# Optimization experiments

Hardware: AMD Instinct MI355X
Metric: run time of the kernel (lower is better)

Reference implementation:

```python
import jax, jax.numpy as jnp
import numpy as np

EMB, NH, NG, T_MAX = 2048, 16, 4, 2048
HD = EMB // NH          # 128
HPG = NH // NG          # 4
B, T = 2, 2048


def _rope_tables(t):
    inv_freq = 1.0 / (10000.0 ** (jnp.arange(0, HD, 2, dtype=jnp.float32) / HD))
    freqs = jnp.outer(jnp.arange(t, dtype=jnp.float32), inv_freq)  # [t, HD//2]
    return jnp.cos(freqs), jnp.sin(freqs)


def _apply_rope(x, cos, sin):
    # x: [..., t, HD], interleaved pairs (0::2 real, 1::2 imag)
    x1 = x[..., 0::2]
    x2 = x[..., 1::2]
    r1 = x1 * cos - x2 * sin
    r2 = x1 * sin + x2 * cos
    return jnp.stack([r1, r2], axis=-1).reshape(x.shape)


def setup_inputs() -> dict:
    key = jax.random.key(0)
    ks = jax.random.split(key, 5)
    s = 0.02
    return {
        "x": jax.random.normal(ks[0], (B, T, EMB), dtype=jnp.float32),
        "Wq": jax.random.normal(ks[1], (EMB, EMB), dtype=jnp.float32) * s,
        "Wk": jax.random.normal(ks[2], (NG * HD, EMB), dtype=jnp.float32) * s,
        "Wv": jax.random.normal(ks[3], (NG * HD, EMB), dtype=jnp.float32) * s,
        "Wo": jax.random.normal(ks[4], (EMB, EMB), dtype=jnp.float32) * s,
    }


def reference(x, Wq, Wk, Wv, Wo):
    b, t, _ = x.shape
    cos, sin = _rope_tables(t)  # [t, HD//2] each; broadcast over batch/heads

    # projections (torch Linear: x @ W.T)
    q = (x @ Wq.T).reshape(b, t, NH, HD).transpose(0, 2, 1, 3)  # [b, NH, t, HD]
    k = (x @ Wk.T).reshape(b, t, NG, HD).transpose(0, 2, 1, 3)  # [b, NG, t, HD]
    v = (x @ Wv.T).reshape(b, t, NG, HD).transpose(0, 2, 1, 3)  # [b, NG, t, HD]

    q = _apply_rope(q, cos, sin)
    k = _apply_rope(k, cos, sin)

    # grouped attention without materializing expanded K/V
    qg = q.reshape(b, NG, HPG, t, HD)                       # [b, g, h, t, d]
    scale = 1.0 / jnp.sqrt(jnp.asarray(HD, dtype=x.dtype))
    scores = jnp.einsum('bghtd,bgsd->bghts', qg, k) * scale  # [b, g, h, t, s]

    causal = jnp.tril(jnp.ones((t, t), dtype=bool))
    scores = jnp.where(causal, scores, jnp.finfo(scores.dtype).min)
    attn = jax.nn.softmax(scores, axis=-1)

    out = jnp.einsum('bghts,bgsd->bghtd', attn, v)           # [b, g, h, t, d]
    out = out.reshape(b, NH, t, HD).transpose(0, 2, 1, 3).reshape(b, t, EMB)
    return out @ Wo.T
```

## Files before the change

kernel.cpp:

```cpp
#include <hip/hip_runtime.h>
#include <stdint.h>
#include <math.h>

#define EMB 2048
#define NHq 16
#define NGk 4
#define HD 128
#define Bb 2
#define Tt 2048
#define MROWS (Bb*Tt)
#define QKVN 3072
#define NQT 32

typedef __bf16 bf16x8 __attribute__((ext_vector_type(8)));
typedef float f32x4 __attribute__((ext_vector_type(4)));
typedef unsigned short u16;
typedef unsigned int u32;

__device__ __forceinline__ u16 f2bf(float f) {
    unsigned int u = __float_as_uint(f);
    u += 0x7fff + ((u >> 16) & 1);
    return (u16)(u >> 16);
}

__device__ __forceinline__ u32 cvt_pk_bf16(float lo, float hi) {
    u32 r;
    asm("v_cvt_pk_bf16_f32 %0, %1, %2" : "=v"(r) : "v"(lo), "v"(hi));
    return r;
}

#define GLOAD_LDS16(g, l) \
    __builtin_amdgcn_global_load_lds((const __attribute__((address_space(1))) void*)(g), \
                                     (__attribute__((address_space(3))) void*)(l), 16, 0, 0)

__global__ void cast_bf16_kernel(const float* __restrict__ src, u16* __restrict__ dst, int n4) {
    int i = blockIdx.x * blockDim.x + threadIdx.x;
    if (i < n4) {
        float4 v = reinterpret_cast<const float4*>(src)[i];
        ushort4 o;
        o.x = f2bf(v.x); o.y = f2bf(v.y); o.z = f2bf(v.z); o.w = f2bf(v.w);
        reinterpret_cast<ushort4*>(dst)[i] = o;
    }
}

__global__ void rope_tables_kernel(float* __restrict__ ctab, float* __restrict__ stab) {
    int t = blockIdx.x, i = threadIdx.x;
    float inv = powf(10000.f, -2.f * (float)i / (float)HD);
    float ang = (float)t * inv;
    ctab[t * 64 + i] = cosf(ang);
    stab[t * 64 + i] = sinf(ang);
}

__global__ void rope_kernel(const float* __restrict__ lin, const float* __restrict__ ctab,
                            const float* __restrict__ stab, u16* __restrict__ out,
                            int coloff, int nh, float scale) {
    int i = threadIdx.x;
    int tt = blockIdx.x * 4 + threadIdx.y;
    int h = blockIdx.y, b = blockIdx.z;
    const float2 xv = *reinterpret_cast<const float2*>(
        &lin[((size_t)(b * Tt + tt)) * QKVN + coloff + h * HD + 2 * i]);
    float c = ctab[tt * 64 + i], s = stab[tt * 64 + i];
    ushort2 o;
    o.x = f2bf((xv.x * c - xv.y * s) * scale);
    o.y = f2bf((xv.x * s + xv.y * c) * scale);
    *reinterpret_cast<ushort2*>(&out[(((size_t)(b * nh + h)) * Tt + tt) * HD + 2 * i]) = o;
}

__global__ void vtrans_kernel(const float* __restrict__ lin, u16* __restrict__ vt) {
    int tx = threadIdx.x, dy = threadIdx.y;
    int tt = blockIdx.x * 64 + tx;
    int g = blockIdx.y, b = blockIdx.z;
    int ttp = (tt & ~31) | (((tt & 15) << 1) | ((tt >> 4) & 1));
    const float* src = &lin[((size_t)(b * Tt + tt)) * QKVN + EMB + NGk * HD + g * HD];
    u16* dst = &vt[(((size_t)(b * NGk + g)) * HD) * Tt + ttp];
    #pragma unroll
    for (int k = 0; k < 16; ++k) {
        int d = dy + k * 8;
        dst[(size_t)d * Tt] = f2bf(src[d]);
    }
}

__global__ __launch_bounds__(256) void gemm_bt(const u16* __restrict__ A, const u16* __restrict__ W,
                                               float* __restrict__ C, int M, int N, int K) {
    __shared__ u16 Atile[128 * 32];
    __shared__ u16 Btile[128 * 32];
    const int brow = blockIdx.x * 128;
    const int bcol = blockIdx.y * 128;
    const int t = threadIdx.x;
    const int w = t >> 6, l = t & 63;
    const int lr = l & 15, lq = l >> 4;
    const int wr = (w >> 1) * 64, wc = (w & 1) * 64;
    f32x4 acc[4][4] = {};
    const int nkt = K >> 5;
    for (int kt = 0; kt < nkt; ++kt) {
        const int k0 = kt * 32;
        #pragma unroll
        for (int i = 0; i < 2; ++i) {
            int f = i * 256 + t;
            int row = f >> 2, cb = (f & 3) * 8;
            GLOAD_LDS16(A + (size_t)(brow + row) * K + k0 + cb, &Atile[(i * 256 + w * 64) * 8]);
            GLOAD_LDS16(W + (size_t)(bcol + row) * K + k0 + cb, &Btile[(i * 256 + w * 64) * 8]);
        }
        __syncthreads();
        bf16x8 a[4], b[4];
        #pragma unroll
        for (int m = 0; m < 4; ++m)
            a[m] = *reinterpret_cast<const bf16x8*>(&Atile[(wr + m * 16 + lr) * 32 + lq * 8]);
        #pragma unroll
        for (int n = 0; n < 4; ++n)
            b[n] = *reinterpret_cast<const bf16x8*>(&Btile[(wc + n * 16 + lr) * 32 + lq * 8]);
        #pragma unroll
        for (int m = 0; m < 4; ++m)
            #pragma unroll
            for (int n = 0; n < 4; ++n)
                acc[m][n] = __builtin_amdgcn_mfma_f32_16x16x32_bf16(a[m], b[n], acc[m][n], 0, 0, 0);
        __syncthreads();
    }
    #pragma unroll
    for (int m = 0; m < 4; ++m)
        #pragma unroll
        for (int n = 0; n < 4; ++n)
            #pragma unroll
            for (int r = 0; r < 4; ++r)
                C[(size_t)(brow + wr + m * 16 + lq * 4 + r) * N + bcol + wc + n * 16 + lr] = acc[m][n][r];
}

__global__ __launch_bounds__(512) void flash_attn(const u16* __restrict__ Q, const u16* __restrict__ K,
                                                  const u16* __restrict__ Vt, u16* __restrict__ Out) {
    __shared__ __align__(16) char smem[73728];
    u16* KldsBase = (u16*)smem;
    u16* VldsBase = (u16*)(smem + 32768);
    const int ilo = blockIdx.x;
    const int ihi = NQT - 1 - ilo;
    const int h = blockIdx.y;
    const int b = blockIdx.z;
    const int g = h >> 2;
    const int t = threadIdx.x;
    const int w = t >> 6, l = t & 63;
    const int wq = w & 3, half = w >> 2;
    const int lr = l & 15, lq = l >> 4;
    char* Pw = smem + 65536 + w * 1024;

    const size_t qhead = ((size_t)(b * NHq + h)) * Tt;
    const size_t qblo = (qhead + ilo * 64 + wq * 16) * HD;
    const size_t qbhi = (qhead + ihi * 64 + wq * 16) * HD;
    bf16x8 qfl[4], qfh[4];
    #pragma unroll
    for (int d = 0; d < 4; ++d) {
        qfl[d] = *reinterpret_cast<const bf16x8*>(&Q[qblo + (size_t)lr * HD + d * 32 + lq * 8]);
        qfh[d] = *reinterpret_cast<const bf16x8*>(&Q[qbhi + (size_t)lr * HD + d * 32 + lq * 8]);
    }
    bf16x8 ones;
    #pragma unroll
    for (int j = 0; j < 8; ++j) ones[j] = (__bf16)1.0f;

    f32x4 ol[8] = {}, oh[8] = {};
    f32x4 lsl = {}, lsh = {};

    const int qlo0 = ilo * 64 + wq * 16 + lq * 4;
    const int qhi0 = ihi * 64 + wq * 16 + lq * 4;
    const size_t kbase  = ((size_t)(b * NGk + g)) * Tt * HD;
    const size_t vtbase = ((size_t)(b * NGk + g)) * HD * Tt;
    const int nkt = NQT - ilo;

    int kofs[2], vofs[2];
    #pragma unroll
    for (int j = 0; j < 2; ++j) {
        int krow = j * 32 + w * 4 + (l >> 4);
        kofs[j] = krow * HD + (((l & 15) ^ (krow & 7)) * 8);
        int vrow = j * 64 + w * 8 + (l >> 3);
        vofs[j] = vrow * (int)Tt + (((l & 7) ^ (vrow & 7)) * 8);
    }

    #pragma unroll
    for (int j = 0; j < 2; ++j) {
        GLOAD_LDS16(K + kbase + kofs[j], KldsBase + (j * 512 + w * 64) * 8);
        GLOAD_LDS16(Vt + vtbase + vofs[j], VldsBase + (j * 512 + w * 64) * 8);
    }
    int cur = 0;

    for (int kt = 0; kt < nkt; ++kt) {
        const int kp0 = kt * 64;
        __syncthreads();
        if (kt + 1 < nkt) {
            #pragma unroll
            for (int j = 0; j < 2; ++j) {
                GLOAD_LDS16(K + kbase + (size_t)(kp0 + 64) * HD + kofs[j],
                            KldsBase + (cur ^ 1) * 8192 + (j * 512 + w * 64) * 8);
                GLOAD_LDS16(Vt + vtbase + (kp0 + 64) + vofs[j],
                            VldsBase + (cur ^ 1) * 8192 + (j * 512 + w * 64) * 8);
            }
        }
        const char* Kb = smem + cur * 16384;
        const char* Vb = smem + 32768 + cur * 16384;

        const bool lo_act = (kt <= ilo);
        f32x4 sl[2] = {}, sh[2] = {};
        __builtin_amdgcn_s_setprio(1);
        #pragma unroll
        for (int ct = 0; ct < 2; ++ct) {
            #pragma unroll
            for (int d = 0; d < 4; ++d) {
                int row = half * 32 + ct * 16 + lr;
                int bo = row * 256 + ((d * 64 + lq * 16) ^ ((row & 7) << 4));
                bf16x8 kf = *reinterpret_cast<const bf16x8*>(Kb + bo);
                if (lo_act) sl[ct] = __builtin_amdgcn_mfma_f32_16x16x32_bf16(qfl[d], kf, sl[ct], 0, 0, 0);
                sh[ct] = __builtin_amdgcn_mfma_f32_16x16x32_bf16(qfh[d], kf, sh[ct], 0, 0, 0);
            }
        }
        __builtin_amdgcn_s_setprio(0);

        {
            const bool diag = (kt == nkt - 1);
            float e[2][4];
            #pragma unroll
            for (int ct = 0; ct < 2; ++ct)
                #pragma unroll
                for (int r = 0; r < 4; ++r) {
                    float v = sh[ct][r];
                    if (diag && (kp0 + half * 32 + ct * 16 + lr > qhi0 + r)) v = -1e30f;
                    e[ct][r] = exp2f(v);
                }
            #pragma unroll
            for (int r = 0; r < 4; ++r) {
                int row = lq * 4 + r;
                int bo = row * 64 + (((lr >> 2) ^ (row & 3)) << 4) + (lr & 3) * 4;
                *reinterpret_cast<u32*>(Pw + bo) = cvt_pk_bf16(e[0][r], e[1][r]);
            }
        }
        bf16x8 pfh = *reinterpret_cast<const bf16x8*>(Pw + lr * 64 + ((lq ^ (lr & 3)) << 4));
        bf16x8 pfl;
        if (lo_act) {
            const bool diag = (kt == ilo);
            float e[2][4];
            #pragma unroll
            for (int ct = 0; ct < 2; ++ct)
                #pragma unroll
                for (int r = 0; r < 4; ++r) {
                    float v = sl[ct][r];
                    if (diag && (kp0 + half * 32 + ct * 16 + lr > qlo0 + r)) v = -1e30f;
                    e[ct][r] = exp2f(v);
                }
            #pragma unroll
            for (int r = 0; r < 4; ++r) {
                int row = lq * 4 + r;
                int bo = row * 64 + (((lr >> 2) ^ (row & 3)) << 4) + (lr & 3) * 4;
                *reinterpret_cast<u32*>(Pw + bo) = cvt_pk_bf16(e[0][r], e[1][r]);
            }
            pfl = *reinterpret_cast<const bf16x8*>(Pw + lr * 64 + ((lq ^ (lr & 3)) << 4));
        }

        __builtin_amdgcn_s_setprio(1);
        #pragma unroll
        for (int n = 0; n < 8; ++n) {
            int vrow = n * 16 + lr;
            int bv = vrow * 128 + ((half * 64 + lq * 16) ^ ((vrow & 7) << 4));
            bf16x8 vf = *reinterpret_cast<const bf16x8*>(Vb + bv);
            oh[n] = __builtin_amdgcn_mfma_f32_16x16x32_bf16(pfh, vf, oh[n], 0, 0, 0);
            if (lo_act) ol[n] = __builtin_amdgcn_mfma_f32_16x16x32_bf16(pfl, vf, ol[n], 0, 0, 0);
        }
        lsh = __builtin_amdgcn_mfma_f32_16x16x32_bf16(pfh, ones, lsh, 0, 0, 0);
        if (lo_act) lsl = __builtin_amdgcn_mfma_f32_16x16x32_bf16(pfl, ones, lsl, 0, 0, 0);
        __builtin_amdgcn_s_setprio(0);
        cur ^= 1;
    }

    __syncthreads();
    float* Osh = (float*)smem;
    float* Lsh = (float*)(smem + 65536);
    if (half == 1) {
        #pragma unroll
        for (int n = 0; n < 8; ++n)
            #pragma unroll
            for (int r = 0; r < 4; ++r) {
                int row = lq * 4 + r, col = n * 16 + lr;
                Osh[(wq * 32 + row) * 128 + col] = oh[n][r];
                Osh[(wq * 32 + 16 + row) * 128 + col] = ol[n][r];
            }
        if (lr == 0) {
            #pragma unroll
            for (int r = 0; r < 4; ++r) {
                Lsh[wq * 32 + lq * 4 + r] = lsh[r];
                Lsh[wq * 32 + 16 + lq * 4 + r] = lsl[r];
            }
        }
    }
    __syncthreads();
    if (half == 0) {
        float invh[4], invl[4];
        #pragma unroll
        for (int r = 0; r < 4; ++r) {
            invh[r] = 1.f / (lsh[r] + Lsh[wq * 32 + lq * 4 + r]);
            invl[r] = 1.f / (lsl[r] + Lsh[wq * 32 + 16 + lq * 4 + r]);
        }
        const size_t obase = ((size_t)b * Tt) * EMB + (size_t)h * HD;
        #pragma unroll
        for (int n = 0; n < 8; ++n)
            #pragma unroll
            for (int r = 0; r < 4; ++r) {
                int row = lq * 4 + r, col = n * 16 + lr;
                float vh = oh[n][r] + Osh[(wq * 32 + row) * 128 + col];
                float vl = ol[n][r] + Osh[(wq * 32 + 16 + row) * 128 + col];
                int rh = ihi * 64 + wq * 16 + row;
                int rl = ilo * 64 + wq * 16 + row;
                Out[obase + (size_t)rh * EMB + col] = f2bf(vh * invh[r]);
                Out[obase + (size_t)rl * EMB + col] = f2bf(vl * invl[r]);
            }
    }
}

extern "C" void kernel_launch(void* const* d_in, const int* in_sizes, int n_in,
                              void* d_out, int out_size, void* d_ws, size_t ws_size,
                              hipStream_t stream) {
    (void)in_sizes; (void)n_in; (void)out_size; (void)ws_size;
    const float* x  = (const float*)d_in[0];
    const float* Wq = (const float*)d_in[1];
    const float* Wk = (const float*)d_in[2];
    const float* Wv = (const float*)d_in[3];
    const float* Wo = (const float*)d_in[4];
    float* out = (float*)d_out;

    char* ws = (char*)d_ws;
    size_t off = 0;
    auto alloc = [&](size_t bytes) { char* p = ws + off; off += (bytes + 255) & ~(size_t)255; return p; };

    u16* w_bf    = (u16*)alloc((size_t)(QKVN * EMB + EMB * EMB) * 2);
    u16* x_bf    = (u16*)alloc((size_t)MROWS * EMB * 2);
    float* qkv_lin = (float*)alloc((size_t)MROWS * QKVN * 4);
    u16* Qb      = (u16*)alloc((size_t)Bb * NHq * Tt * HD * 2);
    u16* Kb      = (u16*)alloc((size_t)Bb * NGk * Tt * HD * 2);
    u16* Vtb     = (u16*)alloc((size_t)Bb * NGk * HD * Tt * 2);
    float* ctab  = (float*)alloc((size_t)Tt * 64 * 4);
    float* stab  = (float*)alloc((size_t)Tt * 64 * 4);
    u16* attnout = (u16*)qkv_lin;

    u16* wq_bf = w_bf;
    u16* wk_bf = w_bf + (size_t)EMB * EMB;
    u16* wv_bf = wk_bf + (size_t)NGk * HD * EMB;
    u16* wo_bf = wv_bf + (size_t)NGk * HD * EMB;

    cast_bf16_kernel<<<(MROWS * EMB / 4 + 255) / 256, 256, 0, stream>>>(x, x_bf, MROWS * EMB / 4);
    cast_bf16_kernel<<<(EMB * EMB / 4 + 255) / 256, 256, 0, stream>>>(Wq, wq_bf, EMB * EMB / 4);
    cast_bf16_kernel<<<(NGk * HD * EMB / 4 + 255) / 256, 256, 0, stream>>>(Wk, wk_bf, NGk * HD * EMB / 4);
    cast_bf16_kernel<<<(NGk * HD * EMB / 4 + 255) / 256, 256, 0, stream>>>(Wv, wv_bf, NGk * HD * EMB / 4);
    cast_bf16_kernel<<<(EMB * EMB / 4 + 255) / 256, 256, 0, stream>>>(Wo, wo_bf, EMB * EMB / 4);
    rope_tables_kernel<<<Tt, 64, 0, stream>>>(ctab, stab);

    gemm_bt<<<dim3(MROWS / 128, QKVN / 128), 256, 0, stream>>>(x_bf, w_bf, qkv_lin, MROWS, QKVN, EMB);

    const float qscale = 1.44269504088896f / sqrtf((float)HD);
    rope_kernel<<<dim3(Tt / 4, NHq, Bb), dim3(64, 4), 0, stream>>>(qkv_lin, ctab, stab, Qb, 0, NHq, qscale);
    rope_kernel<<<dim3(Tt / 4, NGk, Bb), dim3(64, 4), 0, stream>>>(qkv_lin, ctab, stab, Kb, EMB, NGk, 1.0f);
    vtrans_kernel<<<dim3(Tt / 64, NGk, Bb), dim3(64, 8), 0, stream>>>(qkv_lin, Vtb);

    flash_attn<<<dim3(NQT / 2, NHq, Bb), 512, 0, stream>>>(Qb, Kb, Vtb, attnout);

    gemm_bt<<<dim3(MROWS / 128, EMB / 128), 256, 0, stream>>>(attnout, wo_bf, out, MROWS, EMB, EMB);
}
```

Before: 266.9 us.

## Store QKV projection in bf16 and merge weight casts and rope launches

The QKV GEMM now writes bf16 instead of fp32, which halves the intermediate write and the reads in the rope and V-transpose kernels. The four weight cast launches become a single kernel, and the Q and K rope launches become one. Flash-attention block order is reversed for batch 1, presumably to balance causal work across the batches. Rounding the projection to bf16 before RoPE adds a small precision change.

```diff
diff --git a/kernel.cpp b/kernel.cpp
--- a/kernel.cpp
+++ b/kernel.cpp
@@ -22,7 +22,9 @@
     u += 0x7fff + ((u >> 16) & 1);
     return (u16)(u >> 16);
 }
-
+__device__ __forceinline__ float bf2f(u16 u) {
+    return __uint_as_float(((u32)u) << 16);
+}
 __device__ __forceinline__ u32 cvt_pk_bf16(float lo, float hi) {
     u32 r;
     asm("v_cvt_pk_bf16_f32 %0, %1, %2" : "=v"(r) : "v"(lo), "v"(hi));
@@ -43,6 +45,21 @@
     }
 }
 
+__global__ void wcast_kernel(const float* __restrict__ Wq, const float* __restrict__ Wk,
+                             const float* __restrict__ Wv, const float* __restrict__ Wo,
+                             u16* __restrict__ dst) {
+    int i = blockIdx.x * blockDim.x + threadIdx.x;
+    const float* src; int local;
+    if (i < 1048576)      { src = Wq; local = i; }
+    else if (i < 1310720) { src = Wk; local = i - 1048576; }
+    else if (i < 1572864) { src = Wv; local = i - 1310720; }
+    else                  { src = Wo; local = i - 1572864; }
+    float4 v = reinterpret_cast<const float4*>(src)[local];
+    ushort4 o;
+    o.x = f2bf(v.x); o.y = f2bf(v.y); o.z = f2bf(v.z); o.w = f2bf(v.w);
+    reinterpret_cast<ushort4*>(dst)[i] = o;
+}
+
 __global__ void rope_tables_kernel(float* __restrict__ ctab, float* __restrict__ stab) {
     int t = blockIdx.x, i = threadIdx.x;
     float inv = powf(10000.f, -2.f * (float)i / (float)HD);
@@ -51,37 +68,43 @@
     stab[t * 64 + i] = sinf(ang);
 }
 
-__global__ void rope_kernel(const float* __restrict__ lin, const float* __restrict__ ctab,
-                            const float* __restrict__ stab, u16* __restrict__ out,
-                            int coloff, int nh, float scale) {
+__global__ void rope_qk_kernel(const u16* __restrict__ lin, const float* __restrict__ ctab,
+                               const float* __restrict__ stab, u16* __restrict__ Qb,
+                               u16* __restrict__ Kb, float qscale) {
     int i = threadIdx.x;
     int tt = blockIdx.x * 4 + threadIdx.y;
-    int h = blockIdx.y, b = blockIdx.z;
-    const float2 xv = *reinterpret_cast<const float2*>(
-        &lin[((size_t)(b * Tt + tt)) * QKVN + coloff + h * HD + 2 * i]);
+    int hh = blockIdx.y, b = blockIdx.z;
+    int coloff; u16* out; float scale;
+    if (hh < NHq) { coloff = hh * HD; scale = qscale;
+                    out = Qb + (((size_t)(b * NHq + hh)) * Tt + tt) * HD; }
+    else { int g = hh - NHq; coloff = EMB + g * HD; scale = 1.f;
+           out = Kb + (((size_t)(b * NGk + g)) * Tt + tt) * HD; }
+    u32 pair = *reinterpret_cast<const u32*>(&lin[((size_t)(b * Tt + tt)) * QKVN + coloff + 2 * i]);
+    float x1 = bf2f((u16)(pair & 0xffff)), x2 = bf2f((u16)(pair >> 16));
     float c = ctab[tt * 64 + i], s = stab[tt * 64 + i];
     ushort2 o;
-    o.x = f2bf((xv.x * c - xv.y * s) * scale);
-    o.y = f2bf((xv.x * s + xv.y * c) * scale);
-    *reinterpret_cast<ushort2*>(&out[(((size_t)(b * nh + h)) * Tt + tt) * HD + 2 * i]) = o;
-}
-
-__global__ void vtrans_kernel(const float* __restrict__ lin, u16* __restrict__ vt) {
+    o.x = f2bf((x1 * c - x2 * s) * scale);
+    o.y = f2bf((x1 * s + x2 * c) * scale);
+    *reinterpret_cast<ushort2*>(&out[2 * i]) = o;
+}
+
+__global__ void vtrans_kernel(const u16* __restrict__ lin, u16* __restrict__ vt) {
     int tx = threadIdx.x, dy = threadIdx.y;
     int tt = blockIdx.x * 64 + tx;
     int g = blockIdx.y, b = blockIdx.z;
     int ttp = (tt & ~31) | (((tt & 15) << 1) | ((tt >> 4) & 1));
-    const float* src = &lin[((size_t)(b * Tt + tt)) * QKVN + EMB + NGk * HD + g * HD];
+    const u16* src = &lin[((size_t)(b * Tt + tt)) * QKVN + EMB + NGk * HD + g * HD];
     u16* dst = &vt[(((size_t)(b * NGk + g)) * HD) * Tt + ttp];
     #pragma unroll
     for (int k = 0; k < 16; ++k) {
         int d = dy + k * 8;
-        dst[(size_t)d * Tt] = f2bf(src[d]);
-    }
-}
-
+        dst[(size_t)d * Tt] = src[d];
+    }
+}
+
+template<int OUTBF>
 __global__ __launch_bounds__(256) void gemm_bt(const u16* __restrict__ A, const u16* __restrict__ W,
-                                               float* __restrict__ C, int M, int N, int K) {
+                                               void* __restrict__ Cout, int M, int N, int K) {
     __shared__ u16 Atile[128 * 32];
     __shared__ u16 Btile[128 * 32];
     const int brow = blockIdx.x * 128;
@@ -121,8 +144,11 @@
         #pragma unroll
         for (int n = 0; n < 4; ++n)
             #pragma unroll
-            for (int r = 0; r < 4; ++r)
-                C[(size_t)(brow + wr + m * 16 + lq * 4 + r) * N + bcol + wc + n * 16 + lr] = acc[m][n][r];
+            for (int r = 0; r < 4; ++r) {
+                size_t idx = (size_t)(brow + wr + m * 16 + lq * 4 + r) * N + bcol + wc + n * 16 + lr;
+                if (OUTBF) ((u16*)Cout)[idx] = f2bf(acc[m][n][r]);
+                else       ((float*)Cout)[idx] = acc[m][n][r];
+            }
 }
 
 __global__ __launch_bounds__(512) void flash_attn(const u16* __restrict__ Q, const u16* __restrict__ K,
@@ -130,10 +156,10 @@
     __shared__ __align__(16) char smem[73728];
     u16* KldsBase = (u16*)smem;
     u16* VldsBase = (u16*)(smem + 32768);
-    const int ilo = blockIdx.x;
-    const int ihi = NQT - 1 - ilo;
     const int h = blockIdx.y;
     const int b = blockIdx.z;
+    const int ilo = (b == 0) ? blockIdx.x : (NQT / 2 - 1 - blockIdx.x);
+    const int ihi = NQT - 1 - ilo;
     const int g = h >> 2;
     const int t = threadIdx.x;
     const int w = t >> 6, l = t & 63;
@@ -326,34 +352,27 @@
 
     u16* w_bf    = (u16*)alloc((size_t)(QKVN * EMB + EMB * EMB) * 2);
     u16* x_bf    = (u16*)alloc((size_t)MROWS * EMB * 2);
-    float* qkv_lin = (float*)alloc((size_t)MROWS * QKVN * 4);
+    u16* qkv_lin = (u16*)alloc((size_t)MROWS * QKVN * 4);
     u16* Qb      = (u16*)alloc((size_t)Bb * NHq * Tt * HD * 2);
     u16* Kb      = (u16*)alloc((size_t)Bb * NGk * Tt * HD * 2);
     u16* Vtb     = (u16*)alloc((size_t)Bb * NGk * HD * Tt * 2);
     float* ctab  = (float*)alloc((size_t)Tt * 64 * 4);
     float* stab  = (float*)alloc((size_t)Tt * 64 * 4);
-    u16* attnout = (u16*)qkv_lin;
-
-    u16* wq_bf = w_bf;
-    u16* wk_bf = w_bf + (size_t)EMB * EMB;
-    u16* wv_bf = wk_bf + (size_t)NGk * HD * EMB;
-    u16* wo_bf = wv_bf + (size_t)NGk * HD * EMB;
+    u16* attnout = qkv_lin;
+
+    u16* wo_bf = w_bf + (size_t)QKVN * EMB;
 
     cast_bf16_kernel<<<(MROWS * EMB / 4 + 255) / 256, 256, 0, stream>>>(x, x_bf, MROWS * EMB / 4);
-    cast_bf16_kernel<<<(EMB * EMB / 4 + 255) / 256, 256, 0, stream>>>(Wq, wq_bf, EMB * EMB / 4);
-    cast_bf16_kernel<<<(NGk * HD * EMB / 4 + 255) / 256, 256, 0, stream>>>(Wk, wk_bf, NGk * HD * EMB / 4);
-    cast_bf16_kernel<<<(NGk * HD * EMB / 4 + 255) / 256, 256, 0, stream>>>(Wv, wv_bf, NGk * HD * EMB / 4);
-    cast_bf16_kernel<<<(EMB * EMB / 4 + 255) / 256, 256, 0, stream>>>(Wo, wo_bf, EMB * EMB / 4);
+    wcast_kernel<<<(QKVN * EMB + EMB * EMB) / 4 / 256, 256, 0, stream>>>(Wq, Wk, Wv, Wo, w_bf);
     rope_tables_kernel<<<Tt, 64, 0, stream>>>(ctab, stab);
 
-    gemm_bt<<<dim3(MROWS / 128, QKVN / 128), 256, 0, stream>>>(x_bf, w_bf, qkv_lin, MROWS, QKVN, EMB);
+    gemm_bt<1><<<dim3(MROWS / 128, QKVN / 128), 256, 0, stream>>>(x_bf, w_bf, qkv_lin, MROWS, QKVN, EMB);
 
     const float qscale = 1.44269504088896f / sqrtf((float)HD);
-    rope_kernel<<<dim3(Tt / 4, NHq, Bb), dim3(64, 4), 0, stream>>>(qkv_lin, ctab, stab, Qb, 0, NHq, qscale);
-    rope_kernel<<<dim3(Tt / 4, NGk, Bb), dim3(64, 4), 0, stream>>>(qkv_lin, ctab, stab, Kb, EMB, NGk, 1.0f);
+    rope_qk_kernel<<<dim3(Tt / 4, NHq + NGk, Bb), dim3(64, 4), 0, stream>>>(qkv_lin, ctab, stab, Qb, Kb, qscale);
     vtrans_kernel<<<dim3(Tt / 64, NGk, Bb), dim3(64, 8), 0, stream>>>(qkv_lin, Vtb);
 
     flash_attn<<<dim3(NQT / 2, NHq, Bb), 512, 0, stream>>>(Qb, Kb, Vtb, attnout);
 
-    gemm_bt<<<dim3(MROWS / 128, EMB / 128), 256, 0, stream>>>(attnout, wo_bf, out, MROWS, EMB, EMB);
-}
+    gemm_bt<0><<<dim3(MROWS / 128, EMB / 128), 256, 0, stream>>>(attnout, wo_bf, out, MROWS, EMB, EMB);
+}
```

New measurement: 250.6 us. -6.1%, faster.
